# Kernel tuning notes

Hardware: AMD Instinct MI355X
Metric: run time of the kernel (lower is better)

The kernel has to match this reference:

```python
import jax, jax.numpy as jnp
import numpy as np

N, Cin, H, W = 8, 256, 32, 32
Cout, K = 512, 3
DK, DV, NH = 128, 128, 8
DKH, DVH = DK // NH, DV // NH
HW = H * W


def conv2d(x, w, b, stride, pad):
    y = jax.lax.conv_general_dilated(
        x, w, (stride, stride), [(pad, pad), (pad, pad)],
        dimension_numbers=("NCHW", "OIHW", "NCHW"))
    return y + b[None, :, None, None]


def rel_to_abs(x):
    # x: (B, Nh*, L, 2L-1) -> (B, Nh*, L, L) via pad/reshape trick
    B, Nh, L, _ = x.shape
    x = jnp.concatenate([x, jnp.zeros((B, Nh, L, 1), x.dtype)], axis=3)
    flat = x.reshape(B, Nh, L * 2 * L)
    flat = jnp.concatenate([flat, jnp.zeros((B, Nh, L - 1), x.dtype)], axis=2)
    return flat.reshape(B, Nh, L + 1, 2 * L - 1)[:, :, :L, L - 1:]


def relative_logits_1d(q, rel_k, Hq, Wq, case):
    # q: (N, Nh, Hq, Wq, dkh); rel_k: (2*Wq-1, dkh)
    rl = jnp.einsum('bhxyd,md->bhxym', q, rel_k)             # (N,Nh,Hq,Wq,2Wq-1)
    rl = rel_to_abs(rl.reshape(-1, NH * Hq, Wq, 2 * Wq - 1))  # (N,Nh*Hq,Wq,Wq)
    rl = rl.reshape(-1, NH, Hq, Wq, Wq)[:, :, :, None]        # (N,Nh,Hq,1,Wq,Wq)
    rl = jnp.broadcast_to(rl, (rl.shape[0], NH, Hq, Hq, Wq, Wq))  # axes (b,h,x,i,y,j)
    if case == 'w':
        rl = rl.transpose(0, 1, 2, 4, 3, 5)   # (b,h,x,y,i,j)
    else:  # 'h'
        rl = rl.transpose(0, 1, 4, 2, 5, 3)   # (b,h,y,x,j,i)
    return rl.reshape(-1, NH, HW, HW)


def setup_inputs() -> dict:
    key = jax.random.key(0)
    ks = jax.random.split(key, 9)
    s = 0.05
    return {
        'x': jax.random.normal(ks[0], (N, Cin, H, W), jnp.float32),
        'w_out': jax.random.normal(ks[1], (Cout - DV, Cin, K, K), jnp.float32) * s,
        'b_out': jnp.zeros((Cout - DV,), jnp.float32),
        'w_kqv': jax.random.normal(ks[2], (2 * DK + DV, Cin, 1, 1), jnp.float32) * s,
        'b_kqv': jnp.zeros((2 * DK + DV,), jnp.float32),
        'w_attn': jax.random.normal(ks[3], (DV, DV, 1, 1), jnp.float32) * s,
        'b_attn': jnp.zeros((DV,), jnp.float32),
        'key_rel_w': jax.random.normal(ks[4], (2 * W - 1, DKH), jnp.float32),
        'key_rel_h': jax.random.normal(ks[5], (2 * H - 1, DKH), jnp.float32),
    }


def reference(x, w_out, b_out, w_kqv, b_kqv, w_attn, b_attn, key_rel_w, key_rel_h):
    conv_out = conv2d(x, w_out, b_out, 1, (K - 1) // 2)       # (N, Cout-DV, H, W)
    kqv = conv2d(x, w_kqv, b_kqv, 1, 0)                       # (N, 2DK+DV, H, W)
    k, q, v = jnp.split(kqv, [DK, 2 * DK], axis=1)
    q = q * (DKH ** -0.5)
    q5 = q.reshape(N, NH, DKH, H, W)
    flat_q = q5.reshape(N, NH, DKH, HW)
    flat_k = k.reshape(N, NH, DKH, HW)
    flat_v = v.reshape(N, NH, DVH, HW)
    logits = jnp.einsum('bhdm,bhdn->bhmn', flat_q, flat_k)    # (N,NH,HW,HW)
    qt = q5.transpose(0, 1, 3, 4, 2)                          # (N,NH,H,W,dkh)
    rl_w = relative_logits_1d(qt, key_rel_w, H, W, 'w')
    rl_h = relative_logits_1d(qt.transpose(0, 1, 3, 2, 4), key_rel_h, W, H, 'h')
    logits = logits + rl_h + rl_w
    weights = jax.nn.softmax(logits, axis=-1)
    attn = jnp.einsum('bhmn,bhdn->bhmd', weights, flat_v)     # (N,NH,HW,DVH)
    # faithful to torch: raw reshape (N,NH,HW,DVH)->(N,NH,DVH,H,W)->(N,DV,H,W)
    attn = attn.reshape(N, DV, H, W)
    attn = conv2d(attn, w_attn, b_attn, 1, 0)
    return jnp.concatenate([conv_out, attn], axis=1)
```

## Files before the change

### kernel.cpp

```cpp
#include <hip/hip_runtime.h>
#include <hip/hip_bf16.h>


typedef short v8s __attribute__((ext_vector_type(8)));
typedef float v4f __attribute__((ext_vector_type(4)));

#define WB2_US   0u
#define WK2_US   884736u
#define WA2_US   983040u
#define KRWB_US  999424u
#define KRHB_US  1000448u
#define XC_US    1001472u
#define ART2_US  3368960u

#define KS_US    0u
#define QS_US    1048576u
#define VTS_US   2097152u
#define ART1_US  7340032u

#define QSCALE 0.360673760f
#define SHIFT2 17.3123405f

__device__ __forceinline__ unsigned short f2bs(float f) {
  __hip_bfloat16 h = __float2bfloat16(f);
  return *reinterpret_cast<unsigned short*>(&h);
}

__global__ __launch_bounds__(256) void prep_kernel(
    const float* __restrict__ w_out, const float* __restrict__ w_kqv,
    const float* __restrict__ w_attn, const float* __restrict__ krw,
    const float* __restrict__ krh, unsigned short* __restrict__ ws) {
  int i = blockIdx.x * 256 + threadIdx.x;
  if (i < 884736) {
    int j = i & 7, l = (i >> 3) & 63, kc = (i >> 9) & 7, nt = (i >> 12) & 3;
    int r = i >> 14; int coG = r % 6, t = r / 6;
    int co = coG * 64 + nt * 16 + (l & 15);
    int ci = kc * 32 + (l >> 4) * 8 + j;
    ws[WB2_US + i] = f2bs(w_out[(size_t)co * 2304 + ci * 9 + t]);
  } else if (i < 983040) {
    int o = i - 884736;
    int j = o & 7, l = (o >> 3) & 63, kc = (o >> 9) & 7, nt = (o >> 12) & 3;
    int coG = o >> 14;
    int co = coG * 64 + nt * 16 + (l & 15);
    int ci = kc * 32 + (l >> 4) * 8 + j;
    ws[WK2_US + o] = f2bs(w_kqv[co * 256 + ci]);
  } else if (i < 999424) {
    int o = i - 983040;
    int j = o & 7, l = (o >> 3) & 63, kc = (o >> 9) & 3, nt = (o >> 11) & 3;
    int coG = o >> 13;
    int co = coG * 64 + nt * 16 + (l & 15);
    int ci = kc * 32 + (l >> 4) * 8 + j;
    ws[WA2_US + o] = f2bs(w_attn[co * 128 + ci]);
  } else if (i < 1000448) {
    int j = i - 999424; int c = j >> 4, d = j & 15;
    ws[KRWB_US + j] = (c < 63) ? f2bs(krw[c * 16 + d]) : (unsigned short)0;
  } else if (i < 1001472) {
    int j = i - 1000448; int c = j >> 4, d = j & 15;
    ws[KRHB_US + j] = (c < 63) ? f2bs(krh[c * 16 + d]) : (unsigned short)0;
  }
}

__global__ __launch_bounds__(256) void zero_xc_kernel(unsigned short* __restrict__ xc) {
  int i = blockIdx.x * 256 + threadIdx.x;
  uint4 z = {0u, 0u, 0u, 0u};
  ((uint4*)xc)[i] = z;
}

__global__ __launch_bounds__(256) void xt_kernel(
    const float* __restrict__ x, unsigned short* __restrict__ xc) {
  __shared__ float t[64][65];
  int tid = threadIdx.x; int pl = tid & 63, cg = tid >> 6;
  int pos0 = blockIdx.x * 64, ci0 = blockIdx.y * 64, b = blockIdx.z;
  const float* xb = x + ((size_t)(b * 256 + ci0)) * 1024 + pos0;
#pragma unroll
  for (int i = 0; i < 16; ++i) {
    int ci_l = cg * 16 + i;
    t[ci_l][pl] = xb[(size_t)ci_l * 1024 + pl];
  }
  __syncthreads();
#pragma unroll
  for (int i = 0; i < 16; ++i) {
    int pos_l = cg * 16 + i;
    int pos = pos0 + pos_l;
    int y = (pos >> 5) + 1, xx = (pos & 31) + 1;
    int ci = ci0 + pl;
    xc[((size_t)((b * 8 + (ci >> 5)) * 34 + y) * 34 + xx) * 32 + (ci & 31)] =
        f2bs(t[pl][pos_l]);
  }
}

__global__ __launch_bounds__(256) void kqv_mfma(
    const unsigned short* __restrict__ xc, const unsigned short* __restrict__ wk2,
    const float* __restrict__ bkqv, unsigned short* __restrict__ dq) {
  int tid = threadIdx.x;
  int lane = tid & 63; int il = lane & 15, q = lane >> 4;
  int wv = tid >> 6; int mh = wv >> 1, nh = wv & 1;
  int m0 = blockIdx.x * 64, coG = blockIdx.y;
  int b = m0 >> 10, pos0 = m0 & 1023;
  int row0 = pos0 >> 5;
  v4f acc[2][2];
#pragma unroll
  for (int mi = 0; mi < 2; ++mi)
#pragma unroll
    for (int ni = 0; ni < 2; ++ni) acc[mi][ni] = (v4f){0.f, 0.f, 0.f, 0.f};

  int pix[2];
#pragma unroll
  for (int mi = 0; mi < 2; ++mi)
    pix[mi] = (row0 + mh + 1) * 34 + (mi * 16 + il + 1);
  const unsigned short* bt = wk2 + (size_t)coG * 16384 + lane * 8;

#pragma unroll 4
  for (int kc = 0; kc < 8; ++kc) {
    v8s af[2], bf[2];
#pragma unroll
    for (int ni = 0; ni < 2; ++ni)
      bf[ni] = *(const v8s*)(bt + ((nh * 2 + ni) * 8 + kc) * 512);
#pragma unroll
    for (int mi = 0; mi < 2; ++mi)
      af[mi] = *(const v8s*)(xc + ((size_t)(b * 8 + kc) * 1156 + pix[mi]) * 32 + q * 8);
#pragma unroll
    for (int mi = 0; mi < 2; ++mi)
#pragma unroll
      for (int ni = 0; ni < 2; ++ni)
        acc[mi][ni] = __builtin_amdgcn_mfma_f32_16x16x32_bf16(
            af[mi], bf[ni], acc[mi][ni], 0, 0, 0);
  }
  int co0 = coG * 64;
#pragma unroll
  for (int ni = 0; ni < 2; ++ni) {
    int nt = nh * 2 + ni;
    int cob = co0 + nt * 16;
    int co = cob + il;
    float bias = bkqv[co];
    int cls = cob >> 7;
    int h = (cob >> 4) & 7;
    size_t bh = (size_t)(b * 8 + h);
#pragma unroll
    for (int mi = 0; mi < 2; ++mi) {
      int mt = mh * 2 + mi;
      int pos = pos0 + mt * 16 + q * 4;
      v4f a = acc[mi][ni];
#pragma unroll
      for (int r = 0; r < 4; ++r) {
        float v = a[r] + bias;
        int p = pos + r;
        if (cls == 0)      dq[KS_US + bh * 16384 + p * 16 + il] = f2bs(v);
        else if (cls == 1) dq[QS_US + bh * 16384 + p * 16 + il] = f2bs(v * QSCALE);
        else               dq[VTS_US + bh * 16384 + ((p >> 5) * 16 + il) * 32 + (p & 31)] = f2bs(v);
      }
    }
  }
}

__global__ __launch_bounds__(256) void attn_mfma(
    unsigned short* __restrict__ dq, const unsigned short* __restrict__ krwb,
    const unsigned short* __restrict__ krhb, unsigned short* __restrict__ wsart) {
  __shared__ float lds[4][2448];
  int tid = threadIdx.x; int w = tid >> 6, lane = tid & 63;
  int il = lane & 15, q = lane >> 4;
  int bh = blockIdx.y; int b = bh >> 3, h = bh & 7;
  int m0 = blockIdx.x * 64 + w * 16;
  int my = m0 >> 5, mxb = m0 & 31;
  float* pw = lds[w];
  float* ph = pw + 1024;
  unsigned short* pl = (unsigned short*)(ph + 1088);

  const v8s z8 = {0, 0, 0, 0, 0, 0, 0, 0};
  const v4f z4 = {0.f, 0.f, 0.f, 0.f};

  const unsigned short* qrow = dq + QS_US + (size_t)bh * 16384 + (m0 + il) * 16;
  v8s qa = *(const v8s*)(qrow + (q & 1) * 8);
  qa = (q < 2) ? qa : z8;

#pragma unroll
  for (int nt = 0; nt < 4; ++nt) {
    int c = nt * 16 + il;
    v8s bw = *(const v8s*)(krwb + c * 16 + (q & 1) * 8);
    v8s bhh = *(const v8s*)(krhb + c * 16 + (q & 1) * 8);
    bw = (q < 2) ? bw : z8;
    bhh = (q < 2) ? bhh : z8;
    v4f pwc = __builtin_amdgcn_mfma_f32_16x16x32_bf16(qa, bw, z4, 0, 0, 0);
    v4f phc = __builtin_amdgcn_mfma_f32_16x16x32_bf16(qa, bhh, z4, 0, 0, 0);
#pragma unroll
    for (int r = 0; r < 4; ++r) {
      pw[(q * 4 + r) * 64 + c] = pwc[r];
      ph[(q * 4 + r) * 68 + c] = phc[r] - SHIFT2;
    }
  }
  __builtin_amdgcn_wave_barrier();

  float pwv[2][4];
#pragma unroll
  for (int nt2 = 0; nt2 < 2; ++nt2)
#pragma unroll
    for (int r = 0; r < 4; ++r)
      pwv[nt2][r] = pw[il * 64 + (nt2 * 16 + q * 4 + r) - mxb - il + 31];

  v4f oacc = z4;
  float sacc = 0.f;
  const unsigned short* kbase = dq + KS_US + (size_t)bh * 16384;
  const unsigned short* vbase = dq + VTS_US + (size_t)bh * 16384;

  for (int ny = 0; ny < 32; ++ny) {
    float phv = ph[il * 68 + (ny - my + 31)];
    v4f s[2];
#pragma unroll
    for (int nt2 = 0; nt2 < 2; ++nt2) {
      v8s kb = *(const v8s*)(kbase + (ny * 32 + nt2 * 16 + il) * 16 + (q & 1) * 8);
      kb = (q < 2) ? kb : z8;
      s[nt2] = __builtin_amdgcn_mfma_f32_16x16x32_bf16(kb, qa, z4, 0, 0, 0);
    }
#pragma unroll
    for (int nt2 = 0; nt2 < 2; ++nt2) {
      float p[4];
#pragma unroll
      for (int r = 0; r < 4; ++r) {
        float t = s[nt2][r] + pwv[nt2][r] + phv;
        p[r] = exp2f(t);
        sacc += p[r];
      }
      uint2 pk;
      pk.x = (unsigned)f2bs(p[0]) | ((unsigned)f2bs(p[1]) << 16);
      pk.y = (unsigned)f2bs(p[2]) | ((unsigned)f2bs(p[3]) << 16);
      *(uint2*)(pl + il * 40 + nt2 * 16 + q * 4) = pk;
    }
    __builtin_amdgcn_wave_barrier();
    v8s pf = *(const v8s*)(pl + il * 40 + q * 8);
    v8s vb = *(const v8s*)(vbase + (ny * 16 + il) * 32 + q * 8);
    oacc = __builtin_amdgcn_mfma_f32_16x16x32_bf16(pf, vb, oacc, 0, 0, 0);
    __builtin_amdgcn_wave_barrier();
  }

  sacc += __shfl_xor(sacc, 16);
  sacc += __shfl_xor(sacc, 32);

  unsigned short* abase = (b < 6) ? (dq + ART1_US + (size_t)b * 131072)
                                  : (wsart + (size_t)(b - 6) * 131072);
#pragma unroll
  for (int r = 0; r < 4; ++r) {
    float sr = __shfl(sacc, q * 4 + r);
    int m = m0 + q * 4 + r;
    int c = h * 16 + (m >> 6);
    int pp = (m & 63) * 16 + il;
    abase[((c >> 5) * 1024 + pp) * 32 + (c & 31)] = f2bs(oacc[r] / sr);
  }
}

__global__ __launch_bounds__(256) void attn_out_mfma(
    const unsigned short* __restrict__ dq, const unsigned short* __restrict__ wsart,
    const unsigned short* __restrict__ wa2, const float* __restrict__ ba,
    float* __restrict__ out) {
  int tid = threadIdx.x;
  int lane = tid & 63; int il = lane & 15, q = lane >> 4;
  int wv = tid >> 6; int mh = wv >> 1, nh = wv & 1;
  int m0 = blockIdx.x * 64, coG = blockIdx.y;
  int b = m0 >> 10, pp0 = m0 & 1023;
  const unsigned short* ab = (b < 6) ? (dq + ART1_US + (size_t)b * 131072)
                                     : (wsart + (size_t)(b - 6) * 131072);
  const unsigned short* bt = wa2 + (size_t)coG * 8192 + lane * 8;
  v4f acc[2][2];
#pragma unroll
  for (int mi = 0; mi < 2; ++mi)
#pragma unroll
    for (int ni = 0; ni < 2; ++ni) acc[mi][ni] = (v4f){0.f, 0.f, 0.f, 0.f};
#pragma unroll
  for (int kc = 0; kc < 4; ++kc) {
    v8s af[2], bf[2];
#pragma unroll
    for (int ni = 0; ni < 2; ++ni)
      bf[ni] = *(const v8s*)(bt + ((nh * 2 + ni) * 4 + kc) * 512);
#pragma unroll
    for (int mi = 0; mi < 2; ++mi)
      af[mi] = *(const v8s*)(ab + (kc * 1024 + pp0 + (mh * 2 + mi) * 16 + il) * 32 + q * 8);
#pragma unroll
    for (int mi = 0; mi < 2; ++mi)
#pragma unroll
      for (int ni = 0; ni < 2; ++ni)
        acc[mi][ni] = __builtin_amdgcn_mfma_f32_16x16x32_bf16(
            af[mi], bf[ni], acc[mi][ni], 0, 0, 0);
  }
  int co0 = coG * 64;
#pragma unroll
  for (int ni = 0; ni < 2; ++ni) {
    int co = co0 + (nh * 2 + ni) * 16 + il;
    float bias = ba[co];
#pragma unroll
    for (int mi = 0; mi < 2; ++mi) {
      int mt = mh * 2 + mi;
      v4f a = acc[mi][ni];
      float4 v; v.x = a[0] + bias; v.y = a[1] + bias;
      v.z = a[2] + bias; v.w = a[3] + bias;
      *(float4*)(out + ((size_t)(b * 512 + 384 + co)) * 1024 + pp0 + mt * 16 + q * 4) = v;
    }
  }
}

__global__ __launch_bounds__(512) void conv_mfma(
    const unsigned short* __restrict__ xc, const unsigned short* __restrict__ wb2,
    const float* __restrict__ bo, float* __restrict__ out) {
  __shared__ unsigned short xcs[2][6656];
  int tid = threadIdx.x;
  int lane = tid & 63; int il = lane & 15, q = lane >> 4;
  int wv = tid >> 6; int mh = wv >> 1, nh = wv & 1;
  int bx = blockIdx.x, nset = blockIdx.y;
  int b = bx & 7, pt = bx >> 3;
  int pos0 = pt * 128, y0 = pt * 4;
  const unsigned short* xb = xc + ((size_t)(b * 8) * 1156 + y0 * 34) * 32;

  v4f acc[2][3];
#pragma unroll
  for (int mi = 0; mi < 2; ++mi)
#pragma unroll
    for (int j = 0; j < 3; ++j) acc[mi][j] = (v4f){0.f, 0.f, 0.f, 0.f};

  auto stageX = [&](int buf, int kc) {
    const unsigned short* src = xb + (size_t)kc * 36992;
#pragma unroll
    for (int t = 0; t < 2; ++t) {
      int s = wv + t * 8;
      if (s < 13) {
        int C = s * 64 + lane;
        int row = C / 136, rem = C % 136;
        int qv = rem / 34, xx = rem % 34;
        const unsigned short* g = src + ((row * 136 + xx * 4 + qv) << 3);
        __builtin_amdgcn_global_load_lds(
            (const __attribute__((address_space(1))) void*)g,
            (__attribute__((address_space(3))) void*)(&xcs[buf][s * 512]),
            16, 0, 0);
      }
    }
  };

  auto wfrag = [&](int tap, int kc, int j) -> v8s {
    int nfg = nset * 6 + nh * 3 + j;
    int coG = nfg >> 2, nt = nfg & 3;
    return *(const v8s*)(wb2 +
        ((size_t)(((tap * 6 + coG) * 4 + nt) * 8 + kc) * 512 + lane * 8));
  };

  stageX(0, 0);
  v8s bS[3][3];
#pragma unroll
  for (int j = 0; j < 3; ++j) bS[0][j] = wfrag(0, 0, j);
#pragma unroll
  for (int j = 0; j < 3; ++j) bS[1][j] = wfrag(1, 0, j);
  __syncthreads();

  for (int kc = 0; kc < 8; ++kc) {
    int buf = kc & 1;
    if (kc < 7) stageX(buf ^ 1, kc + 1);
#pragma unroll
    for (int tap = 0; tap < 9; ++tap) {
      if (tap < 7 || kc < 7) {
        int t2 = tap + 2, k2 = kc;
        if (t2 >= 9) { t2 -= 9; ++k2; }
#pragma unroll
        for (int j = 0; j < 3; ++j) bS[(tap + 2) % 3][j] = wfrag(t2, k2, j);
      }
      int ky = tap / 3, kx = tap % 3;
      v8s af[2];
#pragma unroll
      for (int mi = 0; mi < 2; ++mi)
        af[mi] = *(const v8s*)&xcs[buf][((mh + ky) * 4 + q) * 272 +
                                        (mi * 16 + kx + il) * 8];
#pragma unroll
      for (int mi = 0; mi < 2; ++mi)
#pragma unroll
        for (int j = 0; j < 3; ++j)
          acc[mi][j] = __builtin_amdgcn_mfma_f32_16x16x32_bf16(
              af[mi], bS[tap % 3][j], acc[mi][j], 0, 0, 0);
    }
    __syncthreads();
  }

  int co0 = nset * 96;
#pragma unroll
  for (int j = 0; j < 3; ++j) {
    int co = co0 + (nh * 3 + j) * 16 + il;
    float bias = bo[co];
#pragma unroll
    for (int mi = 0; mi < 2; ++mi) {
      v4f a = acc[mi][j];
      float4 v; v.x = a[0] + bias; v.y = a[1] + bias;
      v.z = a[2] + bias; v.w = a[3] + bias;
      *(float4*)(out + ((size_t)(b * 512 + co)) * 1024 +
                 pos0 + mh * 32 + mi * 16 + q * 4) = v;
    }
  }
}

extern "C" void kernel_launch(void* const* d_in, const int* in_sizes, int n_in,
                              void* d_out, int out_size, void* d_ws, size_t ws_size,
                              hipStream_t stream) {
  const float* x      = (const float*)d_in[0];
  const float* b_out  = (const float*)d_in[2];
  const float* b_kqv  = (const float*)d_in[4];
  const float* b_attn = (const float*)d_in[6];
  const float* krw    = (const float*)d_in[7];
  const float* krh    = (const float*)d_in[8];
  unsigned short* ws = (unsigned short*)d_ws;
  float* out = (float*)d_out;
  unsigned short* dq = (unsigned short*)d_out;

  prep_kernel<<<3912, 256, 0, stream>>>(
      (const float*)d_in[1], (const float*)d_in[3], (const float*)d_in[5],
      krw, krh, ws);
  zero_xc_kernel<<<1156, 256, 0, stream>>>(ws + XC_US);
  xt_kernel<<<dim3(16, 4, 8), 256, 0, stream>>>(x, ws + XC_US);
  kqv_mfma<<<dim3(128, 6), 256, 0, stream>>>(
      ws + XC_US, ws + WK2_US, b_kqv, dq);
  attn_mfma<<<dim3(16, 64), 256, 0, stream>>>(
      dq, ws + KRWB_US, ws + KRHB_US, ws + ART2_US);
  attn_out_mfma<<<dim3(128, 2), 256, 0, stream>>>(
      dq, ws + ART2_US, ws + WA2_US, b_attn, out);
  conv_mfma<<<dim3(64, 4), 512, 0, stream>>>(
      ws + XC_US, ws + WB2_US, b_out, out);
}
```

Measured before the change: 166.8 us.

## Retile 3x3 conv to smaller blocks, contiguous weight layout, prefetch attention K/V

The conv weight prep is reordered so each output-channel fragment's taps and channel chunks are contiguous, which turns weight fragment loads into simple strided pointer increments. The conv kernel now uses 256-thread blocks covering 2 image rows instead of 4, with less LDS per block. That doubles the grid and sets launch bounds to allow two blocks per CU, aiming at better occupancy and load balance. Separately, the attention loop now loads next-iteration K and V fragments into registers one step ahead, to hide global-load latency behind the MFMA and exp work, at the cost of extra registers and more halo re-reads of input rows.

```diff
diff --git a/kernel.cpp b/kernel.cpp
--- a/kernel.cpp
+++ b/kernel.cpp
@@ -32,11 +32,13 @@
     const float* __restrict__ krh, unsigned short* __restrict__ ws) {
   int i = blockIdx.x * 256 + threadIdx.x;
   if (i < 884736) {
-    int j = i & 7, l = (i >> 3) & 63, kc = (i >> 9) & 7, nt = (i >> 12) & 3;
-    int r = i >> 14; int coG = r % 6, t = r / 6;
+    int j = i & 7, l = (i >> 3) & 63;
+    int r = i >> 9;
+    int tap = r % 9; int r2 = r / 9;
+    int kc = r2 & 7, nt = (r2 >> 3) & 3, coG = r2 >> 5;
     int co = coG * 64 + nt * 16 + (l & 15);
     int ci = kc * 32 + (l >> 4) * 8 + j;
-    ws[WB2_US + i] = f2bs(w_out[(size_t)co * 2304 + ci * 9 + t]);
+    ws[WB2_US + i] = f2bs(w_out[(size_t)co * 2304 + ci * 9 + tap]);
   } else if (i < 983040) {
     int o = i - 884736;
     int j = o & 7, l = (o >> 3) & 63, kc = (o >> 9) & 7, nt = (o >> 12) & 3;
@@ -202,15 +204,23 @@
   const unsigned short* kbase = dq + KS_US + (size_t)bh * 16384;
   const unsigned short* vbase = dq + VTS_US + (size_t)bh * 16384;
 
+  v8s kb0 = *(const v8s*)(kbase + (il) * 16 + (q & 1) * 8);
+  v8s kb1 = *(const v8s*)(kbase + (16 + il) * 16 + (q & 1) * 8);
+  v8s vb0 = *(const v8s*)(vbase + (il) * 32 + q * 8);
+
   for (int ny = 0; ny < 32; ++ny) {
+    v8s kc0 = (q < 2) ? kb0 : z8;
+    v8s kc1 = (q < 2) ? kb1 : z8;
+    v8s vcur = vb0;
+    if (ny < 31) {
+      kb0 = *(const v8s*)(kbase + ((ny + 1) * 32 + il) * 16 + (q & 1) * 8);
+      kb1 = *(const v8s*)(kbase + ((ny + 1) * 32 + 16 + il) * 16 + (q & 1) * 8);
+      vb0 = *(const v8s*)(vbase + ((ny + 1) * 16 + il) * 32 + q * 8);
+    }
     float phv = ph[il * 68 + (ny - my + 31)];
     v4f s[2];
-#pragma unroll
-    for (int nt2 = 0; nt2 < 2; ++nt2) {
-      v8s kb = *(const v8s*)(kbase + (ny * 32 + nt2 * 16 + il) * 16 + (q & 1) * 8);
-      kb = (q < 2) ? kb : z8;
-      s[nt2] = __builtin_amdgcn_mfma_f32_16x16x32_bf16(kb, qa, z4, 0, 0, 0);
-    }
+    s[0] = __builtin_amdgcn_mfma_f32_16x16x32_bf16(kc0, qa, z4, 0, 0, 0);
+    s[1] = __builtin_amdgcn_mfma_f32_16x16x32_bf16(kc1, qa, z4, 0, 0, 0);
 #pragma unroll
     for (int nt2 = 0; nt2 < 2; ++nt2) {
       float p[4];
@@ -227,8 +237,7 @@
     }
     __builtin_amdgcn_wave_barrier();
     v8s pf = *(const v8s*)(pl + il * 40 + q * 8);
-    v8s vb = *(const v8s*)(vbase + (ny * 16 + il) * 32 + q * 8);
-    oacc = __builtin_amdgcn_mfma_f32_16x16x32_bf16(pf, vb, oacc, 0, 0, 0);
+    oacc = __builtin_amdgcn_mfma_f32_16x16x32_bf16(pf, vcur, oacc, 0, 0, 0);
     __builtin_amdgcn_wave_barrier();
   }
 
@@ -296,16 +305,16 @@
   }
 }
 
-__global__ __launch_bounds__(512) void conv_mfma(
-    const unsigned short* __restrict__ xc, const unsigned short* __restrict__ wb2,
+__global__ __launch_bounds__(256, 2) void conv_mfma(
+    const unsigned short* __restrict__ xc, const unsigned short* __restrict__ wb3,
     const float* __restrict__ bo, float* __restrict__ out) {
-  __shared__ unsigned short xcs[2][6656];
+  __shared__ unsigned short xcs[2][4608];
   int tid = threadIdx.x;
   int lane = tid & 63; int il = lane & 15, q = lane >> 4;
   int wv = tid >> 6; int mh = wv >> 1, nh = wv & 1;
   int bx = blockIdx.x, nset = blockIdx.y;
   int b = bx & 7, pt = bx >> 3;
-  int pos0 = pt * 128, y0 = pt * 4;
+  int pos0 = pt * 64, y0 = pt * 2;
   const unsigned short* xb = xc + ((size_t)(b * 8) * 1156 + y0 * 34) * 32;
 
   v4f acc[2][3];
@@ -313,13 +322,21 @@
   for (int mi = 0; mi < 2; ++mi)
 #pragma unroll
     for (int j = 0; j < 3; ++j) acc[mi][j] = (v4f){0.f, 0.f, 0.f, 0.f};
+
+  const unsigned short* wp[3];
+#pragma unroll
+  for (int j = 0; j < 3; ++j) {
+    int nfg = nset * 6 + nh * 3 + j;
+    int coG = nfg >> 2, nt = nfg & 3;
+    wp[j] = wb3 + (size_t)(coG * 4 + nt) * 36864 + lane * 8;
+  }
 
   auto stageX = [&](int buf, int kc) {
     const unsigned short* src = xb + (size_t)kc * 36992;
 #pragma unroll
-    for (int t = 0; t < 2; ++t) {
-      int s = wv + t * 8;
-      if (s < 13) {
+    for (int t = 0; t < 3; ++t) {
+      int s = wv + t * 4;
+      if (s < 9) {
         int C = s * 64 + lane;
         int row = C / 136, rem = C % 136;
         int qv = rem / 34, xx = rem % 34;
@@ -332,19 +349,12 @@
     }
   };
 
-  auto wfrag = [&](int tap, int kc, int j) -> v8s {
-    int nfg = nset * 6 + nh * 3 + j;
-    int coG = nfg >> 2, nt = nfg & 3;
-    return *(const v8s*)(wb2 +
-        ((size_t)(((tap * 6 + coG) * 4 + nt) * 8 + kc) * 512 + lane * 8));
-  };
-
   stageX(0, 0);
   v8s bS[3][3];
 #pragma unroll
-  for (int j = 0; j < 3; ++j) bS[0][j] = wfrag(0, 0, j);
-#pragma unroll
-  for (int j = 0; j < 3; ++j) bS[1][j] = wfrag(1, 0, j);
+  for (int j = 0; j < 3; ++j) bS[0][j] = *(const v8s*)(wp[j]);
+#pragma unroll
+  for (int j = 0; j < 3; ++j) bS[1][j] = *(const v8s*)(wp[j] + 512);
   __syncthreads();
 
   for (int kc = 0; kc < 8; ++kc) {
@@ -352,11 +362,11 @@
     if (kc < 7) stageX(buf ^ 1, kc + 1);
 #pragma unroll
     for (int tap = 0; tap < 9; ++tap) {
-      if (tap < 7 || kc < 7) {
-        int t2 = tap + 2, k2 = kc;
-        if (t2 >= 9) { t2 -= 9; ++k2; }
-#pragma unroll
-        for (int j = 0; j < 3; ++j) bS[(tap + 2) % 3][j] = wfrag(t2, k2, j);
+      int it = kc * 9 + tap;
+      if (it < 70) {
+#pragma unroll
+        for (int j = 0; j < 3; ++j)
+          bS[(tap + 2) % 3][j] = *(const v8s*)(wp[j] + (size_t)(it + 2) * 512);
       }
       int ky = tap / 3, kx = tap % 3;
       v8s af[2];
@@ -414,6 +424,6 @@
       dq, ws + KRWB_US, ws + KRHB_US, ws + ART2_US);
   attn_out_mfma<<<dim3(128, 2), 256, 0, stream>>>(
       dq, ws + ART2_US, ws + WA2_US, b_attn, out);
-  conv_mfma<<<dim3(64, 4), 512, 0, stream>>>(
+  conv_mfma<<<dim3(128, 4), 256, 0, stream>>>(
       ws + XC_US, ws + WB2_US, b_out, out);
 }
```

Result: faster. 160.7 us (-3.6%).
